# Performance work log

Measured on AMD Instinct MI355X. Metric: run time of the kernel, lower is better.

The kernel has to match this reference:

```python
import jax, jax.numpy as jnp
import numpy as np
import math

NUM_HEADS = 8
HIDDEN = 128  # per-head dim == model dim (residual stream)
B, S = 4, 2048
LN_EPS = 1e-6
NEG = -1e9


def setup_inputs() -> dict:
    key = jax.random.key(0)
    ks = jax.random.split(key, 7)
    enc = jax.random.normal(ks[0], (B, S, HIDDEN), dtype=jnp.float32)
    mask = jax.random.randint(ks[1], (B, 1, S, S), 0, 2, dtype=jnp.int32)
    sc = 1.0 / math.sqrt(HIDDEN)
    Wq = jax.random.normal(ks[2], (HIDDEN, HIDDEN * NUM_HEADS), dtype=jnp.float32) * sc
    Wk = jax.random.normal(ks[3], (HIDDEN, HIDDEN * NUM_HEADS), dtype=jnp.float32) * sc
    Wv = jax.random.normal(ks[4], (HIDDEN, HIDDEN * NUM_HEADS), dtype=jnp.float32) * sc
    Wo = jax.random.normal(ks[5], (HIDDEN * NUM_HEADS, HIDDEN), dtype=jnp.float32) * sc
    ln_scale = jnp.ones((HIDDEN,), dtype=jnp.float32)
    ln_bias = jnp.zeros((HIDDEN,), dtype=jnp.float32)
    return {"enc": enc, "mask": mask, "Wq": Wq, "Wk": Wk, "Wv": Wv,
            "Wo": Wo, "ln_scale": ln_scale, "ln_bias": ln_bias}


def _layer_norm(x, scale, bias):
    mu = jnp.mean(x, axis=-1, keepdims=True)
    var = jnp.mean(jnp.square(x - mu), axis=-1, keepdims=True)
    return (x - mu) * jax.lax.rsqrt(var + LN_EPS) * scale + bias


def reference(enc, mask, Wq, Wk, Wv, Wo, ln_scale, ln_bias):
    b, s, d = enc.shape
    h = Wq.shape[1] // d
    # projections -> [b, h, s, d]
    def proj(W):
        return jnp.einsum('bsd,de->bse', enc, W).reshape(b, s, h, d).transpose(0, 2, 1, 3)
    Q, K, V = proj(Wq), proj(Wk), proj(Wv)
    scores = jnp.einsum('bhqd,bhkd->bhqk', Q, K) / math.sqrt(d)
    scores = jnp.where(mask == 0, jnp.float32(NEG), scores)
    attn = jax.nn.softmax(scores, axis=-1)  # dropout is identity in eval mode
    out = jnp.einsum('bhqk,bhkd->bhqd', attn, V)
    out = out.transpose(0, 2, 1, 3).reshape(b, s, h * d)
    out = jnp.einsum('bse,ed->bsd', out, Wo)
    out = _layer_norm(out + enc, ln_scale, ln_bias)
    return (out, attn)
```

## Files before the change

kernel.cpp:

```cpp
#include <hip/hip_runtime.h>
#include <hip/hip_bf16.h>
#include <cstdint>
#include <cstddef>

typedef __bf16 bf16;
typedef __bf16 bf16x8 __attribute__((ext_vector_type(8)));
typedef float  f32x4  __attribute__((ext_vector_type(4)));
typedef unsigned int uint32;

#define MFMA16(a, b, c) __builtin_amdgcn_mfma_f32_16x16x32_bf16((a), (b), (c), 0, 0, 0)

static constexpr int Bn = 4, Hn = 8, Sn = 2048, Dn = 128, En = 1024;


__global__ void k_cvt_enc(const float* __restrict__ in, bf16* __restrict__ out) {
    int i = blockIdx.x * 256 + threadIdx.x;
    out[i] = (bf16)in[i];
}

__global__ void k_cvt_w(const float* __restrict__ w, bf16* __restrict__ wt,
                        int dinLog, int doutLog, float scale) {
    int idx = blockIdx.x * 256 + threadIdx.x;
    int n = idx >> dinLog;
    int k = idx & ((1 << dinLog) - 1);
    wt[idx] = (bf16)(w[(k << doutLog) + n] * scale);
}

__global__ void k_bitmask(const int* __restrict__ m, uint32* __restrict__ bits) {
    int idx = blockIdx.x * 256 + threadIdx.x;
    unsigned long long b = __ballot(m[idx] != 0);
    if ((threadIdx.x & 63) == 0) {
        bits[(idx >> 5)]     = (uint32)b;
        bits[(idx >> 5) + 1] = (uint32)(b >> 32);
    }
}


__global__ __launch_bounds__(256) void k_proj(const bf16* __restrict__ encB,
                                              const bf16* __restrict__ wT0,
                                              const bf16* __restrict__ wT1,
                                              const bf16* __restrict__ wT2,
                                              bf16* __restrict__ qb,
                                              bf16* __restrict__ kbuf,
                                              bf16* __restrict__ vt) {
    const int tid = threadIdx.x, w = tid >> 6, lane = tid & 63;
    const int quad = lane >> 4, l15 = lane & 15;
    const int mat = blockIdx.z;
    const int hh  = blockIdx.y;
    const int e0  = hh * 128;
    const int row0 = blockIdx.x * 64 + w * 16;
    const bf16* wT = (mat == 0) ? wT0 : ((mat == 1) ? wT1 : wT2);

    bf16x8 a[4];
#pragma unroll
    for (int kc = 0; kc < 4; kc++)
        a[kc] = *(const bf16x8*)(encB + (row0 + l15) * Dn + kc * 32 + quad * 8);

    f32x4 acc[8];
#pragma unroll
    for (int nt = 0; nt < 8; nt++) { f32x4 z = {0.f, 0.f, 0.f, 0.f}; acc[nt] = z; }

#pragma unroll
    for (int kc = 0; kc < 4; kc++) {
#pragma unroll
        for (int nt = 0; nt < 8; nt++) {
            bf16x8 b = *(const bf16x8*)(wT + (e0 + nt * 16 + l15) * Dn + kc * 32 + quad * 8);
            acc[nt] = MFMA16(a[kc], b, acc[nt]);
        }
    }

    __shared__ bf16 tile[4 * 16 * 128];
#pragma unroll
    for (int nt = 0; nt < 8; nt++)
#pragma unroll
        for (int r = 0; r < 4; r++)
            tile[(w * 16 + quad * 4 + r) * 128 + nt * 16 + l15] = (bf16)acc[nt][r];
    __syncthreads();

    if (mat < 2) {
        bf16* outp = (mat == 0) ? qb : kbuf;
#pragma unroll
        for (int it = 0; it < 4; it++) {
            int rr = it * 4 + quad;
            int s  = blockIdx.x * 64 + w * 16 + rr;
            int bb = s >> 11, sl = s & 2047;
            bf16* dst = outp + (((size_t)(bb * Hn + hh) * Sn + sl) * Dn) + l15 * 8;
            *(uint4*)dst = *(const uint4*)(tile + (w * 16 + rr) * 128 + l15 * 8);
        }
    } else {
        int dr  = tid >> 1;
        int sc0 = (tid & 1) * 32;
        int sg  = blockIdx.x * 64;
        int bb  = sg >> 11, sl0 = sg & 2047;
        unsigned short tmp[32];
#pragma unroll
        for (int i = 0; i < 32; i++) {
            int sl = sc0 + i;
            tmp[i] = *(const unsigned short*)(tile + sl * 128 + dr);
        }
        bf16* dst = vt + ((size_t)(bb * Hn + hh) * Dn + dr) * Sn + sl0 + sc0;
#pragma unroll
        for (int i = 0; i < 4; i++)
            *(uint4*)(dst + i * 8) = *(const uint4*)(tmp + i * 8);
    }
}


__global__ __launch_bounds__(256, 2) void k_attn(const bf16* __restrict__ qb,
                                                 const bf16* __restrict__ kbuf,
                                                 const bf16* __restrict__ vt,
                                                 const uint32* __restrict__ bits,
                                                 float* __restrict__ attn,
                                                 bf16* __restrict__ ob) {
    const int tid = threadIdx.x, w = tid >> 6, lane = tid & 63;
    const int quad = lane >> 4, l15 = lane & 15;
    const int qblk = blockIdx.x;
    const int bh   = blockIdx.y;
    const int bb   = bh >> 3, hh = bh & 7;
    const int qw0  = qblk * 128 + w * 32;

    __shared__ __align__(16) char smem[58368];
    bf16*  Klds = (bf16*)smem;
    bf16*  Vlds = (bf16*)(smem + 17408);
    float* Plds = (float*)(smem + 39936);
    float* Pw   = Plds + w * (32 * 36);

    const bf16* Kbase = kbuf + (size_t)bh * Sn * Dn;
    const bf16* Qbase = qb   + (size_t)bh * Sn * Dn;
    const bf16* Vbase = vt   + (size_t)bh * Dn * Sn;
    const uint32* mbase = bits + (size_t)bb * (Sn * (Sn / 32));
    float* attnbase = attn + (size_t)bh * Sn * Sn;

    bf16x8 aq[2][4];
#pragma unroll
    for (int qs = 0; qs < 2; qs++)
#pragma unroll
        for (int kc = 0; kc < 4; kc++)
            aq[qs][kc] = *(const bf16x8*)(Qbase + (qw0 + qs * 16 + l15) * Dn + kc * 32 + quad * 8);

    float lsum[8];
#pragma unroll
    for (int ri = 0; ri < 8; ri++) lsum[ri] = 0.f;

    for (int kb = 0; kb < Sn / 64; kb++) {
        {
            int krow = tid >> 2, c0 = (tid & 3) * 32;
            const bf16* src = Kbase + (size_t)(kb * 64 + krow) * Dn + c0;
            bf16* dst = Klds + krow * 136 + c0;
#pragma unroll
            for (int i = 0; i < 4; i++)
                *(uint4*)(dst + i * 8) = *(const uint4*)(src + i * 8);
        }
        __syncthreads();

        uint32 mw0[8], mw1[8];
#pragma unroll
        for (int ri = 0; ri < 8; ri++) {
            int q = qw0 + (ri >> 2) * 16 + quad * 4 + (ri & 3);
            uint2 m = *(const uint2*)(mbase + (size_t)q * (Sn / 32) + kb * 2);
            mw0[ri] = m.x; mw1[ri] = m.y;
        }

#pragma unroll
        for (int ct = 0; ct < 4; ct++) {
            f32x4 z = {0.f, 0.f, 0.f, 0.f};
            f32x4 sc0 = z, sc1 = z;
            __builtin_amdgcn_s_setprio(1);
#pragma unroll
            for (int kc = 0; kc < 4; kc++) {
                bf16x8 bk = *(const bf16x8*)(Klds + (ct * 16 + l15) * 136 + kc * 32 + quad * 8);
                sc0 = MFMA16(aq[0][kc], bk, sc0);
                sc1 = MFMA16(aq[1][kc], bk, sc1);
            }
            __builtin_amdgcn_s_setprio(0);
            int sh = (ct & 1) * 16 + l15;
            int hi = ct >> 1;
#pragma unroll
            for (int r = 0; r < 4; r++) {
                uint32 m0 = hi ? mw1[r] : mw0[r];
                float v0 = ((m0 >> sh) & 1u) ? sc0[r] : -1e9f;
                lsum[r] += __expf(v0);
                uint32 m1 = hi ? mw1[4 + r] : mw0[4 + r];
                float v1 = ((m1 >> sh) & 1u) ? sc1[r] : -1e9f;
                lsum[4 + r] += __expf(v1);
            }
        }
        __syncthreads();
    }

    float invl[8];
#pragma unroll
    for (int ri = 0; ri < 8; ri++) {
        float t = lsum[ri];
        t += __shfl_xor(t, 1, 64);
        t += __shfl_xor(t, 2, 64);
        t += __shfl_xor(t, 4, 64);
        t += __shfl_xor(t, 8, 64);
        invl[ri] = (t > 0.f) ? (1.0f / t) : 0.0f;
    }

    f32x4 o[2][8];
#pragma unroll
    for (int qs = 0; qs < 2; qs++)
#pragma unroll
        for (int nt = 0; nt < 8; nt++) { f32x4 z = {0.f, 0.f, 0.f, 0.f}; o[qs][nt] = z; }

    for (int kb = 0; kb < Sn / 64; kb++) {
        {
            int krow = tid >> 2, c0 = (tid & 3) * 32;
            const bf16* src = Kbase + (size_t)(kb * 64 + krow) * Dn + c0;
            bf16* dst = Klds + krow * 136 + c0;
#pragma unroll
            for (int i = 0; i < 4; i++)
                *(uint4*)(dst + i * 8) = *(const uint4*)(src + i * 8);
        }
        {
            int dr = tid >> 1, c0 = (tid & 1) * 32;
            const bf16* src = Vbase + (size_t)dr * Sn + kb * 64 + c0;
            bf16* dst = Vlds + dr * 88 + c0;
#pragma unroll
            for (int i = 0; i < 4; i++)
                *(uint4*)(dst + i * 8) = *(const uint4*)(src + i * 8);
        }
        __syncthreads();

        uint32 mw0[8], mw1[8];
#pragma unroll
        for (int ri = 0; ri < 8; ri++) {
            int q = qw0 + (ri >> 2) * 16 + quad * 4 + (ri & 3);
            uint2 m = *(const uint2*)(mbase + (size_t)q * (Sn / 32) + kb * 2);
            mw0[ri] = m.x; mw1[ri] = m.y;
        }

#pragma unroll
        for (int kt = 0; kt < 2; kt++) {
#pragma unroll
            for (int ct2 = 0; ct2 < 2; ct2++) {
                int ct = kt * 2 + ct2;
                f32x4 z = {0.f, 0.f, 0.f, 0.f};
                f32x4 s0 = z, s1 = z;
                __builtin_amdgcn_s_setprio(1);
#pragma unroll
                for (int kc = 0; kc < 4; kc++) {
                    bf16x8 bk = *(const bf16x8*)(Klds + (ct * 16 + l15) * 136 + kc * 32 + quad * 8);
                    s0 = MFMA16(aq[0][kc], bk, s0);
                    s1 = MFMA16(aq[1][kc], bk, s1);
                }
                __builtin_amdgcn_s_setprio(0);
                int sh = (ct & 1) * 16 + l15;
                int hi = ct >> 1;
#pragma unroll
                for (int r = 0; r < 4; r++) {
                    {
                        uint32 m = hi ? mw1[r] : mw0[r];
                        float v = ((m >> sh) & 1u) ? s0[r] : -1e9f;
                        float il = invl[r];
                        float p = __expf(v) * il + ((il == 0.f) ? (1.0f / 2048.0f) : 0.f);
                        Pw[(quad * 4 + r) * 36 + ct2 * 16 + l15] = p;
                    }
                    {
                        uint32 m = hi ? mw1[4 + r] : mw0[4 + r];
                        float v = ((m >> sh) & 1u) ? s1[r] : -1e9f;
                        float il = invl[4 + r];
                        float p = __expf(v) * il + ((il == 0.f) ? (1.0f / 2048.0f) : 0.f);
                        Pw[(16 + quad * 4 + r) * 36 + ct2 * 16 + l15] = p;
                    }
                }
            }
            bf16x8 ap[2];
#pragma unroll
            for (int qs = 0; qs < 2; qs++) {
                f32x4 p0 = *(const f32x4*)(Pw + (qs * 16 + l15) * 36 + quad * 8);
                f32x4 p1 = *(const f32x4*)(Pw + (qs * 16 + l15) * 36 + quad * 8 + 4);
                float* gd = attnbase + (size_t)(qw0 + qs * 16 + l15) * Sn + kb * 64 + kt * 32 + quad * 8;
                *(f32x4*)gd = p0;
                *(f32x4*)(gd + 4) = p1;
                bf16x8 t;
                t[0] = (bf16)p0[0]; t[1] = (bf16)p0[1]; t[2] = (bf16)p0[2]; t[3] = (bf16)p0[3];
                t[4] = (bf16)p1[0]; t[5] = (bf16)p1[1]; t[6] = (bf16)p1[2]; t[7] = (bf16)p1[3];
                ap[qs] = t;
            }
            __builtin_amdgcn_s_setprio(1);
#pragma unroll
            for (int nt = 0; nt < 8; nt++) {
                bf16x8 bv = *(const bf16x8*)(Vlds + (nt * 16 + l15) * 88 + kt * 32 + quad * 8);
                o[0][nt] = MFMA16(ap[0], bv, o[0][nt]);
                o[1][nt] = MFMA16(ap[1], bv, o[1][nt]);
            }
            __builtin_amdgcn_s_setprio(0);
        }
        __syncthreads();
    }

    bf16* Olds = (bf16*)smem;
    bf16* Ow = Olds + w * (32 * 128);
#pragma unroll
    for (int qs = 0; qs < 2; qs++)
#pragma unroll
        for (int nt = 0; nt < 8; nt++)
#pragma unroll
            for (int r = 0; r < 4; r++)
                Ow[(qs * 16 + quad * 4 + r) * 128 + nt * 16 + l15] = (bf16)o[qs][nt][r];
#pragma unroll
    for (int it = 0; it < 8; it++) {
        int rr = it * 4 + quad;
        int s = qblk * 128 + w * 32 + rr;
        bf16* dst = ob + ((size_t)bb * Sn + s) * En + hh * Dn + l15 * 8;
        *(uint4*)dst = *(const uint4*)(Ow + rr * 128 + l15 * 8);
    }
}


__global__ __launch_bounds__(256) void k_final(const bf16* __restrict__ ob,
                                               const bf16* __restrict__ woT,
                                               const float* __restrict__ enc,
                                               const float* __restrict__ lnsc,
                                               const float* __restrict__ lnbi,
                                               float* __restrict__ out) {
    const int tid = threadIdx.x, w = tid >> 6, lane = tid & 63;
    const int quad = lane >> 4, l15 = lane & 15;
    const int row0 = blockIdx.x * 64 + w * 16;

    f32x4 acc[8];
#pragma unroll
    for (int nt = 0; nt < 8; nt++) { f32x4 z = {0.f, 0.f, 0.f, 0.f}; acc[nt] = z; }

    for (int kc = 0; kc < 32; kc++) {
        bf16x8 a = *(const bf16x8*)(ob + (size_t)(row0 + l15) * En + kc * 32 + quad * 8);
#pragma unroll
        for (int nt = 0; nt < 8; nt++) {
            bf16x8 b = *(const bf16x8*)(woT + (size_t)(nt * 16 + l15) * En + kc * 32 + quad * 8);
            acc[nt] = MFMA16(a, b, acc[nt]);
        }
    }

#pragma unroll
    for (int r = 0; r < 4; r++) {
        int row = row0 + quad * 4 + r;
        float xv[8];
        float s1 = 0.f, s2 = 0.f;
#pragma unroll
        for (int nt = 0; nt < 8; nt++) {
            float xx = acc[nt][r] + enc[(size_t)row * Dn + nt * 16 + l15];
            xv[nt] = xx;
            s1 += xx;
            s2 += xx * xx;
        }
        s1 += __shfl_xor(s1, 1, 64); s2 += __shfl_xor(s2, 1, 64);
        s1 += __shfl_xor(s1, 2, 64); s2 += __shfl_xor(s2, 2, 64);
        s1 += __shfl_xor(s1, 4, 64); s2 += __shfl_xor(s2, 4, 64);
        s1 += __shfl_xor(s1, 8, 64); s2 += __shfl_xor(s2, 8, 64);
        float mu = s1 * (1.0f / 128.0f);
        float var = s2 * (1.0f / 128.0f) - mu * mu;
        float rs = rsqrtf(var + 1e-6f);
#pragma unroll
        for (int nt = 0; nt < 8; nt++) {
            int col = nt * 16 + l15;
            out[(size_t)row * Dn + col] = (xv[nt] - mu) * rs * lnsc[col] + lnbi[col];
        }
    }
}


extern "C" void kernel_launch(void* const* d_in, const int* in_sizes, int n_in,
                              void* d_out, int out_size, void* d_ws, size_t ws_size,
                              hipStream_t stream) {
    (void)in_sizes; (void)n_in; (void)out_size; (void)ws_size;
    const float* enc  = (const float*)d_in[0];
    const int*   mask = (const int*)d_in[1];
    const float* Wq   = (const float*)d_in[2];
    const float* Wk   = (const float*)d_in[3];
    const float* Wv   = (const float*)d_in[4];
    const float* Wo   = (const float*)d_in[5];
    const float* lnsc = (const float*)d_in[6];
    const float* lnbi = (const float*)d_in[7];

    char* ws = (char*)d_ws;
    bf16*   encB = (bf16*)(ws + 0);
    bf16*   WqT  = (bf16*)(ws + 2097152);
    bf16*   WkT  = (bf16*)(ws + 2359296);
    bf16*   WvT  = (bf16*)(ws + 2621440);
    bf16*   WoT  = (bf16*)(ws + 2883584);
    uint32* bits = (uint32*)(ws + 3145728);
    bf16*   QB   = (bf16*)(ws + 5242880);
    bf16*   KB   = (bf16*)(ws + 22020096);
    bf16*   VT   = (bf16*)(ws + 38797312);
    bf16*   OB   = (bf16*)(ws + 55574528);

    float* outp = (float*)d_out;
    float* attn = outp + (size_t)Bn * Sn * Dn;

    k_cvt_enc<<<dim3(4096), dim3(256), 0, stream>>>(enc, encB);
    k_cvt_w<<<dim3(512), dim3(256), 0, stream>>>(Wq, WqT, 7, 10, 0.08838834764831845f);
    k_cvt_w<<<dim3(512), dim3(256), 0, stream>>>(Wk, WkT, 7, 10, 1.0f);
    k_cvt_w<<<dim3(512), dim3(256), 0, stream>>>(Wv, WvT, 7, 10, 1.0f);
    k_cvt_w<<<dim3(512), dim3(256), 0, stream>>>(Wo, WoT, 10, 7, 1.0f);
    k_bitmask<<<dim3(65536), dim3(256), 0, stream>>>(mask, bits);
    k_proj<<<dim3(128, 8, 3), dim3(256), 0, stream>>>(encB, WqT, WkT, WvT, QB, KB, VT);
    k_attn<<<dim3(16, 32), dim3(256), 0, stream>>>(QB, KB, VT, bits, attn, OB);
    k_final<<<dim3(128), dim3(256), 0, stream>>>(OB, WoT, enc, lnsc, lnbi, outp);
}
```

Measured before the change: 898.4 us.

## Read K and V fragments directly from global memory, drop LDS staging and barriers

The attention kernel no longer stages K and V tiles through shared memory. Each wave loads its MFMA B-operands straight from global memory (relying on L1/L2), which removes both per-iteration __syncthreads and shrinks LDS use, and that may allow more blocks per CU. The large attention-probability output is now written with nontemporal stores so it bypasses cache retention. The risk is redundant global and L2 traffic, since all four waves now fetch the same K/V data, and longer load latency in the MFMA loops.

New measurement: 1.047 ms. 16.5% more time.

```diff
diff --git a/kernel.cpp b/kernel.cpp
--- a/kernel.cpp
+++ b/kernel.cpp
@@ -119,11 +119,8 @@
     const int bb   = bh >> 3, hh = bh & 7;
     const int qw0  = qblk * 128 + w * 32;
 
-    __shared__ __align__(16) char smem[58368];
-    bf16*  Klds = (bf16*)smem;
-    bf16*  Vlds = (bf16*)(smem + 17408);
-    float* Plds = (float*)(smem + 39936);
-    float* Pw   = Plds + w * (32 * 36);
+    __shared__ __align__(16) char smem[32768];
+    float* Pw = (float*)(smem + w * 8192);
 
     const bf16* Kbase = kbuf + (size_t)bh * Sn * Dn;
     const bf16* Qbase = qb   + (size_t)bh * Sn * Dn;
@@ -143,16 +140,6 @@
     for (int ri = 0; ri < 8; ri++) lsum[ri] = 0.f;
 
     for (int kb = 0; kb < Sn / 64; kb++) {
-        {
-            int krow = tid >> 2, c0 = (tid & 3) * 32;
-            const bf16* src = Kbase + (size_t)(kb * 64 + krow) * Dn + c0;
-            bf16* dst = Klds + krow * 136 + c0;
-#pragma unroll
-            for (int i = 0; i < 4; i++)
-                *(uint4*)(dst + i * 8) = *(const uint4*)(src + i * 8);
-        }
-        __syncthreads();
-
         uint32 mw0[8], mw1[8];
 #pragma unroll
         for (int ri = 0; ri < 8; ri++) {
@@ -168,7 +155,7 @@
             __builtin_amdgcn_s_setprio(1);
 #pragma unroll
             for (int kc = 0; kc < 4; kc++) {
-                bf16x8 bk = *(const bf16x8*)(Klds + (ct * 16 + l15) * 136 + kc * 32 + quad * 8);
+                bf16x8 bk = *(const bf16x8*)(Kbase + (size_t)(kb * 64 + ct * 16 + l15) * Dn + kc * 32 + quad * 8);
                 sc0 = MFMA16(aq[0][kc], bk, sc0);
                 sc1 = MFMA16(aq[1][kc], bk, sc1);
             }
@@ -185,7 +172,6 @@
                 lsum[4 + r] += __expf(v1);
             }
         }
-        __syncthreads();
     }
 
     float invl[8];
@@ -206,24 +192,6 @@
         for (int nt = 0; nt < 8; nt++) { f32x4 z = {0.f, 0.f, 0.f, 0.f}; o[qs][nt] = z; }
 
     for (int kb = 0; kb < Sn / 64; kb++) {
-        {
-            int krow = tid >> 2, c0 = (tid & 3) * 32;
-            const bf16* src = Kbase + (size_t)(kb * 64 + krow) * Dn + c0;
-            bf16* dst = Klds + krow * 136 + c0;
-#pragma unroll
-            for (int i = 0; i < 4; i++)
-                *(uint4*)(dst + i * 8) = *(const uint4*)(src + i * 8);
-        }
-        {
-            int dr = tid >> 1, c0 = (tid & 1) * 32;
-            const bf16* src = Vbase + (size_t)dr * Sn + kb * 64 + c0;
-            bf16* dst = Vlds + dr * 88 + c0;
-#pragma unroll
-            for (int i = 0; i < 4; i++)
-                *(uint4*)(dst + i * 8) = *(const uint4*)(src + i * 8);
-        }
-        __syncthreads();
-
         uint32 mw0[8], mw1[8];
 #pragma unroll
         for (int ri = 0; ri < 8; ri++) {
@@ -242,7 +210,7 @@
                 __builtin_amdgcn_s_setprio(1);
 #pragma unroll
                 for (int kc = 0; kc < 4; kc++) {
-                    bf16x8 bk = *(const bf16x8*)(Klds + (ct * 16 + l15) * 136 + kc * 32 + quad * 8);
+                    bf16x8 bk = *(const bf16x8*)(Kbase + (size_t)(kb * 64 + ct * 16 + l15) * Dn + kc * 32 + quad * 8);
                     s0 = MFMA16(aq[0][kc], bk, s0);
                     s1 = MFMA16(aq[1][kc], bk, s1);
                 }
@@ -273,8 +241,8 @@
                 f32x4 p0 = *(const f32x4*)(Pw + (qs * 16 + l15) * 36 + quad * 8);
                 f32x4 p1 = *(const f32x4*)(Pw + (qs * 16 + l15) * 36 + quad * 8 + 4);
                 float* gd = attnbase + (size_t)(qw0 + qs * 16 + l15) * Sn + kb * 64 + kt * 32 + quad * 8;
-                *(f32x4*)gd = p0;
-                *(f32x4*)(gd + 4) = p1;
+                __builtin_nontemporal_store(p0, (f32x4*)gd);
+                __builtin_nontemporal_store(p1, (f32x4*)(gd + 4));
                 bf16x8 t;
                 t[0] = (bf16)p0[0]; t[1] = (bf16)p0[1]; t[2] = (bf16)p0[2]; t[3] = (bf16)p0[3];
                 t[4] = (bf16)p1[0]; t[5] = (bf16)p1[1]; t[6] = (bf16)p1[2]; t[7] = (bf16)p1[3];
@@ -283,17 +251,15 @@
             __builtin_amdgcn_s_setprio(1);
 #pragma unroll
             for (int nt = 0; nt < 8; nt++) {
-                bf16x8 bv = *(const bf16x8*)(Vlds + (nt * 16 + l15) * 88 + kt * 32 + quad * 8);
+                bf16x8 bv = *(const bf16x8*)(Vbase + (size_t)(nt * 16 + l15) * Sn + kb * 64 + kt * 32 + quad * 8);
                 o[0][nt] = MFMA16(ap[0], bv, o[0][nt]);
                 o[1][nt] = MFMA16(ap[1], bv, o[1][nt]);
             }
             __builtin_amdgcn_s_setprio(0);
         }
-        __syncthreads();
-    }
-
-    bf16* Olds = (bf16*)smem;
-    bf16* Ow = Olds + w * (32 * 128);
+    }
+
+    bf16* Ow = (bf16*)(smem + w * 8192);
 #pragma unroll
     for (int qs = 0; qs < 2; qs++)
 #pragma unroll
```
